# Optimization experiments

Measured on AMD Instinct MI355X. Metric: run time of the kernel, lower is better.

Reference implementation:

```python
import jax, jax.numpy as jnp
import numpy as np

B, DIM, H, W, HEAD = 8, 512, 32, 32, 8
DH = DIM // HEAD
N = H * W


def setup_inputs() -> dict:
    key = jax.random.key(0)
    ks = jax.random.split(key, 9)
    s = 0.05  # keep conv-weight scale modest so softmax logits are sane
    return {
        "x": jax.random.normal(ks[0], (B, DIM, H, W), jnp.float32),
        "wq_w": jax.random.normal(ks[1], (DIM, DIM), jnp.float32) * s,
        "wq_b": jax.random.normal(ks[2], (DIM,), jnp.float32) * s,
        "wk_w": jax.random.normal(ks[3], (DIM, DIM), jnp.float32) * s,
        "wk_b": jax.random.normal(ks[4], (DIM,), jnp.float32) * s,
        "wv_w": jax.random.normal(ks[5], (DIM, DIM), jnp.float32) * s,
        "wv_b": jax.random.normal(ks[6], (DIM,), jnp.float32) * s,
        "r_h": jax.random.normal(ks[7], (1, HEAD, DH, 1, H), jnp.float32),
        "r_w": jax.random.normal(ks[8], (1, HEAD, DH, W, 1), jnp.float32),
    }


def reference(x, wq_w, wq_b, wk_w, wk_b, wv_w, wv_b, r_h, r_w):
    b, dim, h, w = x.shape
    head = r_h.shape[1]
    dh = dim // head
    n = h * w

    def conv1x1(inp, wgt, bias):
        # 1x1 conv == channel-mixing matmul
        return jnp.einsum('bchw,oc->bohw', inp, wgt) + bias[None, :, None, None]

    q = conv1x1(x, wq_w, wq_b).reshape(b, head, dh, n).transpose(0, 1, 3, 2)  # [b,h,n,d]
    k = conv1x1(x, wk_w, wk_b).reshape(b, head, dh, n)                        # [b,h,d,n]
    v = conv1x1(x, wv_w, wv_b).reshape(b, head, dh, n)                        # [b,h,d,n]

    # relative position term: (1,head,dh,1,H)+(1,head,dh,W,1) -> (1,head,dh,W*H)
    r = (r_h + r_w).reshape(head, dh, n)

    content_position = jnp.einsum('bhnd,hdm->bhnm', q, r)
    content_content = jnp.einsum('bhnd,bhdm->bhnm', q, k)
    # faithful odd reduction: softmax over the whole flattened (head*n*n) per batch row
    energy = (content_content + content_position).reshape(b, -1)
    attention = jax.nn.softmax(energy, axis=-1).reshape(b, head, n, n)

    feature = jnp.einsum('bhdn,bhnm->bhdm', v, attention).reshape(b, dim, h, w)
    # AvgPool2d(kernel=2, stride=2)
    out = feature.reshape(b, dim, h // 2, 2, w // 2, 2).mean(axis=(3, 5))
    return out
```

## Files before the change

kernel.cpp:

```cpp
#include <hip/hip_runtime.h>
#include <hip/hip_bf16.h>
#include <math.h>

#define BB   8
#define DIMC 512
#define HEAD 8
#define DH   64
#define NN   1024
#define HW   32

typedef __attribute__((ext_vector_type(8))) __bf16 bf16x8;
typedef __attribute__((ext_vector_type(4))) float  f32x4;
typedef __attribute__((ext_vector_type(4))) short  short4v;

#define MFMA16(a, b, c) __builtin_amdgcn_mfma_f32_16x16x32_bf16((a), (b), (c), 0, 0, 0)

__device__ __forceinline__ f32x4 mfma_pv(short4v a, short4v b, f32x4 c) {
#if __has_builtin(__builtin_amdgcn_mfma_f32_16x16x16bf16_1k)
    return __builtin_amdgcn_mfma_f32_16x16x16bf16_1k(a, b, c, 0, 0, 0);
#else
    asm volatile("v_mfma_f32_16x16x16_bf16 %0, %1, %2, %0"
                 : "+v"(c) : "v"(a), "v"(b));
    return c;
#endif
}

__device__ __forceinline__ int SW(int row, int col) {
    return (row << 6) + (col ^ ((row & 7) << 3));
}

__device__ __forceinline__ unsigned short bfh(float v) {
    unsigned int u = __float_as_uint(v);
    return (unsigned short)((u + 0x7fffu + ((u >> 16) & 1u)) >> 16);
}
__device__ __forceinline__ float bf2f(unsigned short h) {
    return __uint_as_float(((unsigned int)h) << 16);
}

__global__ __launch_bounds__(256)
void prep_x(const float* __restrict__ x,
            unsigned short* __restrict__ XTh, unsigned short* __restrict__ XTl)
{
    const int tid = threadIdx.x;
    const int nt = blockIdx.x;
    const int ct = blockIdx.y;
    const int b  = blockIdx.z;
    const int c0 = ct << 6, n0 = nt << 6;

    __shared__ float XsT[64][68];

    #pragma unroll
    for (int p = 0; p < 4; ++p) {
        int idx = tid + (p << 8);
        int cr = idx >> 4;
        int nc4 = (idx & 15) << 2;
        float4 v = *(const float4*)&x[((size_t)b * DIMC + c0 + cr) * NN + n0 + nc4];
        XsT[nc4 + 0][cr] = v.x;
        XsT[nc4 + 1][cr] = v.y;
        XsT[nc4 + 2][cr] = v.z;
        XsT[nc4 + 3][cr] = v.w;
    }
    __syncthreads();
    #pragma unroll
    for (int p = 0; p < 4; ++p) {
        int idx = tid + (p << 8);
        int n = idx >> 4;
        int c4 = (idx & 15) << 2;
        float4 v = *(const float4*)&XsT[n][c4];
        float vv[4] = {v.x, v.y, v.z, v.w};
        union { unsigned short u[4]; uint2 w; } ph, pl;
        #pragma unroll
        for (int j = 0; j < 4; ++j) {
            unsigned short hh = bfh(vv[j]);
            ph.u[j] = hh;
            pl.u[j] = bfh(vv[j] - bf2f(hh));
        }
        size_t off = ((size_t)(b * NN + n0 + n)) * DIMC + c0 + c4;
        *(uint2*)&XTh[off] = ph.w;
        *(uint2*)&XTl[off] = pl.w;
    }
}

__global__ __launch_bounds__(256)
void prep_w(const float* __restrict__ wq, const float* __restrict__ wk,
            const float* __restrict__ wv,
            unsigned short* __restrict__ Wh, unsigned short* __restrict__ Wl)
{
    const int z = blockIdx.y;
    const float* src = (z == 0) ? wq : (z == 1) ? wk : wv;
    const size_t zb = (size_t)z * DIMC * DIMC;
    #pragma unroll
    for (int p = 0; p < 4; ++p) {
        size_t i = (size_t)blockIdx.x * 4096 + (p << 10) + (threadIdx.x << 2);
        float4 v = *(const float4*)&src[i];
        float vv[4] = {v.x, v.y, v.z, v.w};
        union { unsigned short u[4]; uint2 w; } ph, pl;
        #pragma unroll
        for (int j = 0; j < 4; ++j) {
            unsigned short hh = bfh(vv[j]);
            ph.u[j] = hh;
            pl.u[j] = bfh(vv[j] - bf2f(hh));
        }
        *(uint2*)&Wh[zb + i] = ph.w;
        *(uint2*)&Wl[zb + i] = pl.w;
    }
}

__global__ __launch_bounds__(256)
void qkv_gemm(const unsigned short* __restrict__ XTh, const unsigned short* __restrict__ XTl,
              const unsigned short* __restrict__ Wh, const unsigned short* __restrict__ Wl,
              const float* __restrict__ wq_b, const float* __restrict__ wk_b,
              const float* __restrict__ wv_b,
              const float* __restrict__ r_h, const float* __restrict__ r_w,
              unsigned short* __restrict__ Qh, unsigned short* __restrict__ Ql,
              unsigned short* __restrict__ Kh, unsigned short* __restrict__ Kl,
              unsigned short* __restrict__ Vh, unsigned short* __restrict__ Vl)
{
    const int tid = threadIdx.x;
    const int z = blockIdx.z, hd = blockIdx.y;
    const int gn = blockIdx.x << 7;
    const int b = gn >> 10, posb = gn & 1023;
    const int oB = hd << 6;
    const int lane = tid & 63, w = tid >> 6;

    __shared__ __align__(16) unsigned short sm[24576];
    unsigned short* Ah = sm;
    unsigned short* Al = sm + 4096;
    unsigned short* Bh = sm + 8192;
    unsigned short* Bl = sm + 16384;

    const float* bias = (z == 0) ? wq_b : (z == 1) ? wk_b : wv_b;
    const unsigned short* wsh = Wh + (size_t)z * DIMC * DIMC + (size_t)oB * DIMC;
    const unsigned short* wsl = Wl + (size_t)z * DIMC * DIMC + (size_t)oB * DIMC;
    const unsigned short* xth = XTh + ((size_t)(b * NN + posb)) * DIMC;
    const unsigned short* xtl = XTl + ((size_t)(b * NN + posb)) * DIMC;

    f32x4 acc[8];
    #pragma unroll
    for (int t = 0; t < 8; ++t) acc[t] = (f32x4){0.f, 0.f, 0.f, 0.f};

    for (int ks = 0; ks < 8; ++ks) {
        const int c0 = ks << 6;
        #pragma unroll
        for (int p = 0; p < 2; ++p) {
            int idx = (p << 8) + tid;
            int row = idx >> 3, col8 = (idx & 7) << 3;
            size_t g = (size_t)row * DIMC + c0 + col8;
            *(float4*)&Ah[SW(row, col8)] = *(const float4*)&wsh[g];
            *(float4*)&Al[SW(row, col8)] = *(const float4*)&wsl[g];
        }
        #pragma unroll
        for (int p = 0; p < 4; ++p) {
            int idx = (p << 8) + tid;
            int row = idx >> 3, col8 = (idx & 7) << 3;
            size_t g = (size_t)row * DIMC + c0 + col8;
            *(float4*)&Bh[SW(row, col8)] = *(const float4*)&xth[g];
            *(float4*)&Bl[SW(row, col8)] = *(const float4*)&xtl[g];
        }
        __syncthreads();

        const int ar = (w << 4) + (lane & 15);
        const int kc = (lane >> 4) << 3;
        bf16x8 ah[2], al[2];
        ah[0] = *(const bf16x8*)&Ah[SW(ar, kc)];
        ah[1] = *(const bf16x8*)&Ah[SW(ar, 32 + kc)];
        al[0] = *(const bf16x8*)&Al[SW(ar, kc)];
        al[1] = *(const bf16x8*)&Al[SW(ar, 32 + kc)];
        #pragma unroll
        for (int t = 0; t < 8; ++t) {
            int br = (t << 4) + (lane & 15);
            #pragma unroll
            for (int s = 0; s < 2; ++s) {
                bf16x8 xh = *(const bf16x8*)&Bh[SW(br, s * 32 + kc)];
                bf16x8 xl = *(const bf16x8*)&Bl[SW(br, s * 32 + kc)];
                acc[t] = MFMA16(ah[s], xh, acc[t]);
                acc[t] = MFMA16(ah[s], xl, acc[t]);
                acc[t] = MFMA16(al[s], xh, acc[t]);
            }
        }
        __syncthreads();
    }

    float* F = (float*)sm;
    #pragma unroll
    for (int t = 0; t < 8; ++t) {
        int n = (t << 4) + (lane & 15);
        #pragma unroll
        for (int r = 0; r < 4; ++r) {
            int o = (w << 4) + ((lane >> 4) << 2) + r;
            F[o * 132 + n] = acc[t][r];
        }
    }
    __syncthreads();

    const size_t bh = (size_t)(b * HEAD + hd);
    if (z != 2) {
        unsigned short* Dh = (z == 0) ? Qh : Kh;
        unsigned short* Dl = (z == 0) ? Ql : Kl;
        #pragma unroll
        for (int p = 0; p < 8; ++p) {
            int idx = (p << 8) + tid;
            int n = idx >> 4, d0 = (idx & 15) << 2;
            union { unsigned short u[4]; uint2 v; } ph, pl;
            #pragma unroll
            for (int i = 0; i < 4; ++i) {
                int d = d0 + i;
                float val = F[d * 132 + n] + bias[oB + d];
                if (z == 1) {
                    int m = posb + n;
                    val += r_h[(size_t)(oB + d) * HW + (m & 31)]
                         + r_w[(size_t)(oB + d) * HW + (m >> 5)];
                }
                unsigned short hh = bfh(val);
                ph.u[i] = hh;
                pl.u[i] = bfh(val - bf2f(hh));
            }
            size_t off = (((size_t)bh * NN + posb + n) << 6) + d0;
            *(uint2*)&Dh[off] = ph.v;
            *(uint2*)&Dl[off] = pl.v;
        }
    } else {
        #pragma unroll
        for (int p = 0; p < 8; ++p) {
            int idx = (p << 8) + tid;
            int d = idx >> 5, n0 = (idx & 31) << 2;
            float4 v = *(const float4*)&F[d * 132 + n0];
            float vv[4] = {v.x, v.y, v.z, v.w};
            float bia = bias[oB + d];
            union { unsigned short u[4]; uint2 w2; } ph, pl;
            #pragma unroll
            for (int j = 0; j < 4; ++j) {
                float val = vv[j] + bia;
                unsigned short hh = bfh(val);
                ph.u[j] = hh;
                pl.u[j] = bfh(val - bf2f(hh));
            }
            size_t off = (((size_t)bh << 6) + d) * NN + posb + n0;
            *(uint2*)&Vh[off] = ph.w2;
            *(uint2*)&Vl[off] = pl.w2;
        }
    }
}

__global__ __launch_bounds__(256, 4)
void stats_kernel(const unsigned short* __restrict__ Qh, const unsigned short* __restrict__ Ql,
                  const unsigned short* __restrict__ Kh, const unsigned short* __restrict__ Kl,
                  float* __restrict__ pstats)
{
    const int tid = threadIdx.x;
    const int mt = blockIdx.x, hd = blockIdx.y, b = blockIdx.z;
    const int bh = b * HEAD + hd;
    const int lane = tid & 63, w = tid >> 6;
    const int r0 = lane & 15, c0 = (lane >> 4) << 3;

    __shared__ float red[512];

    const unsigned short* kh = Kh + (((size_t)bh * NN + (mt << 6)) << 6);
    const unsigned short* kl = Kl + (((size_t)bh * NN + (mt << 6)) << 6);
    bf16x8 kfh[4][2], kfl[4][2];
    #pragma unroll
    for (int t = 0; t < 4; ++t)
        #pragma unroll
        for (int s = 0; s < 2; ++s) {
            int off = (((t << 4) + r0) << 6) + (s << 5) + c0;
            kfh[t][s] = *(const bf16x8*)&kh[off];
            kfl[t][s] = *(const bf16x8*)&kl[off];
        }

    const unsigned short* qh = Qh + (((size_t)bh * NN) << 6);
    const unsigned short* ql = Ql + (((size_t)bh * NN) << 6);

    float m_r = -1e30f, s_r = 0.f;

    for (int nt = 0; nt < 16; ++nt) {
        const int qrow = (nt << 6) + (w << 4) + r0;
        const size_t qb = ((size_t)qrow << 6) + c0;
        bf16x8 ah0 = *(const bf16x8*)&qh[qb];
        bf16x8 ah1 = *(const bf16x8*)&qh[qb + 32];
        bf16x8 al0 = *(const bf16x8*)&ql[qb];
        bf16x8 al1 = *(const bf16x8*)&ql[qb + 32];

        f32x4 sacc[4];
        #pragma unroll
        for (int t = 0; t < 4; ++t) sacc[t] = (f32x4){0.f, 0.f, 0.f, 0.f};
        #pragma unroll
        for (int t = 0; t < 4; ++t) {
            sacc[t] = MFMA16(ah0, kfh[t][0], sacc[t]);
            sacc[t] = MFMA16(ah0, kfl[t][0], sacc[t]);
            sacc[t] = MFMA16(al0, kfh[t][0], sacc[t]);
        }
        #pragma unroll
        for (int t = 0; t < 4; ++t) {
            sacc[t] = MFMA16(ah1, kfh[t][1], sacc[t]);
            sacc[t] = MFMA16(ah1, kfl[t][1], sacc[t]);
            sacc[t] = MFMA16(al1, kfh[t][1], sacc[t]);
        }

        float tmax = -1e30f;
        #pragma unroll
        for (int t = 0; t < 4; ++t)
            #pragma unroll
            for (int r = 0; r < 4; ++r) tmax = fmaxf(tmax, sacc[t][r]);
        float nm = fmaxf(m_r, tmax);
        s_r *= __expf(m_r - nm);
        float tt = 0.f;
        #pragma unroll
        for (int t = 0; t < 4; ++t)
            #pragma unroll
            for (int r = 0; r < 4; ++r) tt += __expf(sacc[t][r] - nm);
        s_r += tt;
        m_r = nm;
    }

    red[tid] = m_r;
    red[256 + tid] = s_r;
    __syncthreads();
    for (int off = 128; off > 0; off >>= 1) {
        if (tid < off) {
            float m2 = red[tid + off], s2 = red[256 + tid + off];
            float M = fmaxf(red[tid], m2);
            red[256 + tid] = red[256 + tid] * __expf(red[tid] - M) + s2 * __expf(m2 - M);
            red[tid] = M;
        }
        __syncthreads();
    }
    if (tid == 0) {
        pstats[((b << 7) + (hd << 4) + mt) * 2 + 0] = red[0];
        pstats[((b << 7) + (hd << 4) + mt) * 2 + 1] = red[256];
    }
}

__global__ __launch_bounds__(128)
void combine_kernel(const float* __restrict__ pstats, float* __restrict__ gstats)
{
    const int b = blockIdx.x, tid = threadIdx.x;
    __shared__ float rm[128], rs[128];
    rm[tid] = pstats[((b << 7) + tid) * 2 + 0];
    rs[tid] = pstats[((b << 7) + tid) * 2 + 1];
    __syncthreads();
    for (int off = 64; off > 0; off >>= 1) {
        if (tid < off) {
            float m2 = rm[tid + off], s2 = rs[tid + off];
            float M = fmaxf(rm[tid], m2);
            rs[tid] = rs[tid] * __expf(rm[tid] - M) + s2 * __expf(m2 - M);
            rm[tid] = M;
        }
        __syncthreads();
    }
    if (tid == 0) { gstats[b * 2] = rm[0]; gstats[b * 2 + 1] = rs[0]; }
}

__global__ __launch_bounds__(256, 2)
void pv_kernel(const unsigned short* __restrict__ Qh, const unsigned short* __restrict__ Ql,
               const unsigned short* __restrict__ Kh, const unsigned short* __restrict__ Kl,
               const unsigned short* __restrict__ Vh, const unsigned short* __restrict__ Vl,
               const float* __restrict__ gstats, float* __restrict__ out)
{
    const int tid = threadIdx.x;
    const int mt = blockIdx.x, hd = blockIdx.y, b = blockIdx.z;
    const int bh = b * HEAD + hd;
    const int lane = tid & 63, w = tid >> 6;
    const int r0 = lane & 15, c0 = (lane >> 4) << 3;

    __shared__ __align__(16) unsigned char smraw[2 * 64 * 65 * 4];
    unsigned short* Vsh = (unsigned short*)smraw;
    unsigned short* Vsl = Vsh + 4096;
    float* F0 = (float*)smraw;
    float* F1 = F0 + 64 * 65;

    const unsigned short* kh = Kh + (((size_t)bh * NN + (mt << 6)) << 6);
    const unsigned short* kl = Kl + (((size_t)bh * NN + (mt << 6)) << 6);
    bf16x8 kfh[4][2], kfl[4][2];
    #pragma unroll
    for (int t = 0; t < 4; ++t)
        #pragma unroll
        for (int s = 0; s < 2; ++s) {
            int off = (((t << 4) + r0) << 6) + (s << 5) + c0;
            kfh[t][s] = *(const bf16x8*)&kh[off];
            kfl[t][s] = *(const bf16x8*)&kl[off];
        }

    const unsigned short* qh = Qh + (((size_t)bh * NN) << 6);
    const unsigned short* ql = Ql + (((size_t)bh * NN) << 6);
    const unsigned short* vh = Vh + (((size_t)bh << 6) * NN);
    const unsigned short* vl = Vl + (((size_t)bh << 6) * NN);

    const float gmax = gstats[b * 2];
    const float ginv = 1.f / gstats[b * 2 + 1];

    f32x4 facc[4][4];
    #pragma unroll
    for (int u = 0; u < 4; ++u)
        #pragma unroll
        for (int t = 0; t < 4; ++t) facc[u][t] = (f32x4){0.f, 0.f, 0.f, 0.f};

    for (int nt = 0; nt < 16; ++nt) {
        const int nB = nt << 6;
        #pragma unroll
        for (int p = 0; p < 2; ++p) {
            int idx = (p << 8) + tid;
            int row = idx >> 3, c8 = (idx & 7) << 3;
            *(float4*)&Vsh[SW(row, c8)] = *(const float4*)&vh[(size_t)row * NN + nB + c8];
            *(float4*)&Vsl[SW(row, c8)] = *(const float4*)&vl[(size_t)row * NN + nB + c8];
        }
        const int qrow = nB + (w << 4) + r0;
        const size_t qb = ((size_t)qrow << 6) + c0;
        bf16x8 ah0 = *(const bf16x8*)&qh[qb];
        bf16x8 ah1 = *(const bf16x8*)&qh[qb + 32];
        bf16x8 al0 = *(const bf16x8*)&ql[qb];
        bf16x8 al1 = *(const bf16x8*)&ql[qb + 32];
        __syncthreads();

        f32x4 sacc[4];
        #pragma unroll
        for (int t = 0; t < 4; ++t) sacc[t] = (f32x4){0.f, 0.f, 0.f, 0.f};
        #pragma unroll
        for (int t = 0; t < 4; ++t) {
            sacc[t] = MFMA16(ah0, kfh[t][0], sacc[t]);
            sacc[t] = MFMA16(ah0, kfl[t][0], sacc[t]);
            sacc[t] = MFMA16(al0, kfh[t][0], sacc[t]);
        }
        #pragma unroll
        for (int t = 0; t < 4; ++t) {
            sacc[t] = MFMA16(ah1, kfh[t][1], sacc[t]);
            sacc[t] = MFMA16(ah1, kfl[t][1], sacc[t]);
            sacc[t] = MFMA16(al1, kfh[t][1], sacc[t]);
        }

        short4v pah[4], pal[4];
        #pragma unroll
        for (int t = 0; t < 4; ++t) {
            union { unsigned short u[4]; short4v v; } Ph, Pl;
            #pragma unroll
            for (int r = 0; r < 4; ++r) {
                float a = __expf(sacc[t][r] - gmax) * ginv;
                unsigned short hh = bfh(a);
                Ph.u[r] = hh;
                Pl.u[r] = bfh(a - bf2f(hh));
            }
            pah[t] = Ph.v;
            pal[t] = Pl.v;
        }

        const int vcol = (w << 4) + ((lane >> 4) << 2);
        #pragma unroll
        for (int u = 0; u < 4; ++u) {
            int vrow = (u << 4) + r0;
            short4v vah = *(const short4v*)&Vsh[SW(vrow, vcol)];
            short4v vbl = *(const short4v*)&Vsl[SW(vrow, vcol)];
            #pragma unroll
            for (int t = 0; t < 4; ++t) {
                facc[u][t] = mfma_pv(vah, pah[t], facc[u][t]);
                facc[u][t] = mfma_pv(vbl, pah[t], facc[u][t]);
                facc[u][t] = mfma_pv(vah, pal[t], facc[u][t]);
            }
        }
        __syncthreads();
    }

    const int fr = (lane >> 4) << 2;
    if (w < 2) {
        float* Fw = (w == 0) ? F0 : F1;
        #pragma unroll
        for (int u = 0; u < 4; ++u)
            #pragma unroll
            for (int t = 0; t < 4; ++t)
                #pragma unroll
                for (int r = 0; r < 4; ++r)
                    Fw[((u << 4) + fr + r) * 65 + (t << 4) + r0] = facc[u][t][r];
    }
    __syncthreads();
    if (w >= 2) {
        float* Fw = (w == 2) ? F0 : F1;
        #pragma unroll
        for (int u = 0; u < 4; ++u)
            #pragma unroll
            for (int t = 0; t < 4; ++t)
                #pragma unroll
                for (int r = 0; r < 4; ++r)
                    Fw[((u << 4) + fr + r) * 65 + (t << 4) + r0] += facc[u][t][r];
    }
    __syncthreads();
    #pragma unroll
    for (int q = 0; q < 4; ++q) {
        int idx = (tid << 2) + q;
        int d = idx >> 4, wo = idx & 15;
        int m0 = wo << 1;
        float v = 0.25f * ((F0[d * 65 + m0]      + F1[d * 65 + m0]) +
                           (F0[d * 65 + m0 + 1]  + F1[d * 65 + m0 + 1]) +
                           (F0[d * 65 + 32 + m0] + F1[d * 65 + 32 + m0]) +
                           (F0[d * 65 + 33 + m0] + F1[d * 65 + 33 + m0]));
        out[(((size_t)(b * DIMC + (hd << 6) + d) << 4) + mt) * 16 + wo] = v;
    }
}

extern "C" void kernel_launch(void* const* d_in, const int* in_sizes, int n_in,
                              void* d_out, int out_size, void* d_ws, size_t ws_size,
                              hipStream_t stream)
{
    const float* x    = (const float*)d_in[0];
    const float* wq_w = (const float*)d_in[1];
    const float* wq_b = (const float*)d_in[2];
    const float* wk_w = (const float*)d_in[3];
    const float* wk_b = (const float*)d_in[4];
    const float* wv_w = (const float*)d_in[5];
    const float* wv_b = (const float*)d_in[6];
    const float* r_h  = (const float*)d_in[7];
    const float* r_w  = (const float*)d_in[8];
    float* out = (float*)d_out;

    const size_t PRN = (size_t)BB * HEAD * NN * DH;
    const size_t WSZ = (size_t)3 * DIMC * DIMC;
    unsigned short* Qh  = (unsigned short*)d_ws;
    unsigned short* Ql  = Qh + PRN;
    unsigned short* Kh  = Ql + PRN;
    unsigned short* Kl  = Kh + PRN;
    unsigned short* Vh  = Kl + PRN;
    unsigned short* Vl  = Vh + PRN;
    unsigned short* XTh = Vl + PRN;
    unsigned short* XTl = XTh + PRN;
    unsigned short* Wh  = XTl + PRN;
    unsigned short* Wl  = Wh + WSZ;
    float* pstats = (float*)(Wl + WSZ);
    float* gstats = pstats + BB * 128 * 2;

    prep_x<<<dim3(16, 8, 8), 256, 0, stream>>>(x, XTh, XTl);
    prep_w<<<dim3(64, 3), 256, 0, stream>>>(wq_w, wk_w, wv_w, Wh, Wl);
    qkv_gemm<<<dim3(64, 8, 3), 256, 0, stream>>>(XTh, XTl, Wh, Wl,
                                                 wq_b, wk_b, wv_b, r_h, r_w,
                                                 Qh, Ql, Kh, Kl, Vh, Vl);
    stats_kernel<<<dim3(16, 8, 8), 256, 0, stream>>>(Qh, Ql, Kh, Kl, pstats);
    combine_kernel<<<dim3(8), 128, 0, stream>>>(pstats, gstats);
    pv_kernel<<<dim3(16, 8, 8), 256, 0, stream>>>(Qh, Ql, Kh, Kl, Vh, Vl, gstats, out);
}
```

Baseline: 256.9 us.

## Fuse softmax stats pass into PV pass with online rescaling and finalize

Replaces the separate stats pass and the PV pass, which both recomputed QK^T, with a single flash-style kernel. It keeps a per-wave running max, rescales the accumulators and writes an unnormalized pooled output plus per-block (max, sum). A small finalize kernel then applies the global softmax normalization per block. This removes one full QK^T recomputation and one read of Q/K, at the cost of extra rescale work, wave shuffles and an additional light kernel that writes pooled data into the reused XTh buffer.

```diff
diff --git a/kernel.cpp b/kernel.cpp
--- a/kernel.cpp
+++ b/kernel.cpp
@@ -242,10 +242,11 @@
     }
 }
 
-__global__ __launch_bounds__(256, 4)
-void stats_kernel(const unsigned short* __restrict__ Qh, const unsigned short* __restrict__ Ql,
-                  const unsigned short* __restrict__ Kh, const unsigned short* __restrict__ Kl,
-                  float* __restrict__ pstats)
+__global__ __launch_bounds__(256, 2)
+void flash_pv(const unsigned short* __restrict__ Qh, const unsigned short* __restrict__ Ql,
+              const unsigned short* __restrict__ Kh, const unsigned short* __restrict__ Kl,
+              const unsigned short* __restrict__ Vh, const unsigned short* __restrict__ Vl,
+              float* __restrict__ pooled, float* __restrict__ pstats)
 {
     const int tid = threadIdx.x;
     const int mt = blockIdx.x, hd = blockIdx.y, b = blockIdx.z;
@@ -253,7 +254,12 @@
     const int lane = tid & 63, w = tid >> 6;
     const int r0 = lane & 15, c0 = (lane >> 4) << 3;
 
-    __shared__ float red[512];
+    __shared__ __align__(16) unsigned char smraw[2 * 64 * 65 * 4];
+    unsigned short* Vsh = (unsigned short*)smraw;
+    unsigned short* Vsl = Vsh + 4096;
+    float* F0 = (float*)smraw;
+    float* F1 = F0 + 64 * 65;
+    __shared__ float bm[4], bs[4];
 
     const unsigned short* kh = Kh + (((size_t)bh * NN + (mt << 6)) << 6);
     const unsigned short* kl = Kl + (((size_t)bh * NN + (mt << 6)) << 6);
@@ -269,16 +275,34 @@
 
     const unsigned short* qh = Qh + (((size_t)bh * NN) << 6);
     const unsigned short* ql = Ql + (((size_t)bh * NN) << 6);
-
-    float m_r = -1e30f, s_r = 0.f;
+    const unsigned short* vh = Vh + (((size_t)bh << 6) * NN);
+    const unsigned short* vl = Vl + (((size_t)bh << 6) * NN);
+
+    float m_w = -1e30f;
+    float s_r = 0.f;
+
+    f32x4 facc[4][4];
+    #pragma unroll
+    for (int u = 0; u < 4; ++u)
+        #pragma unroll
+        for (int t = 0; t < 4; ++t) facc[u][t] = (f32x4){0.f, 0.f, 0.f, 0.f};
 
     for (int nt = 0; nt < 16; ++nt) {
-        const int qrow = (nt << 6) + (w << 4) + r0;
+        const int nB = nt << 6;
+        #pragma unroll
+        for (int p = 0; p < 2; ++p) {
+            int idx = (p << 8) + tid;
+            int row = idx >> 3, c8 = (idx & 7) << 3;
+            *(float4*)&Vsh[SW(row, c8)] = *(const float4*)&vh[(size_t)row * NN + nB + c8];
+            *(float4*)&Vsl[SW(row, c8)] = *(const float4*)&vl[(size_t)row * NN + nB + c8];
+        }
+        const int qrow = nB + (w << 4) + r0;
         const size_t qb = ((size_t)qrow << 6) + c0;
         bf16x8 ah0 = *(const bf16x8*)&qh[qb];
         bf16x8 ah1 = *(const bf16x8*)&qh[qb + 32];
         bf16x8 al0 = *(const bf16x8*)&ql[qb];
         bf16x8 al1 = *(const bf16x8*)&ql[qb + 32];
+        __syncthreads();
 
         f32x4 sacc[4];
         #pragma unroll
@@ -301,32 +325,101 @@
         for (int t = 0; t < 4; ++t)
             #pragma unroll
             for (int r = 0; r < 4; ++r) tmax = fmaxf(tmax, sacc[t][r]);
-        float nm = fmaxf(m_r, tmax);
-        s_r *= __expf(m_r - nm);
-        float tt = 0.f;
-        #pragma unroll
-        for (int t = 0; t < 4; ++t)
-            #pragma unroll
-            for (int r = 0; r < 4; ++r) tt += __expf(sacc[t][r] - nm);
-        s_r += tt;
-        m_r = nm;
-    }
-
-    red[tid] = m_r;
-    red[256 + tid] = s_r;
+        #pragma unroll
+        for (int off = 1; off < 64; off <<= 1)
+            tmax = fmaxf(tmax, __shfl_xor(tmax, off, 64));
+        if (tmax > m_w) {
+            float sc = __expf(m_w - tmax);
+            s_r *= sc;
+            #pragma unroll
+            for (int u = 0; u < 4; ++u)
+                #pragma unroll
+                for (int t = 0; t < 4; ++t) facc[u][t] *= sc;
+            m_w = tmax;
+        }
+
+        short4v pah[4], pal[4];
+        #pragma unroll
+        for (int t = 0; t < 4; ++t) {
+            union { unsigned short u[4]; short4v v; } Ph, Pl;
+            #pragma unroll
+            for (int r = 0; r < 4; ++r) {
+                float a = __expf(sacc[t][r] - m_w);
+                s_r += a;
+                unsigned short hh = bfh(a);
+                Ph.u[r] = hh;
+                Pl.u[r] = bfh(a - bf2f(hh));
+            }
+            pah[t] = Ph.v;
+            pal[t] = Pl.v;
+        }
+
+        const int vcol = (w << 4) + ((lane >> 4) << 2);
+        #pragma unroll
+        for (int u = 0; u < 4; ++u) {
+            int vrow = (u << 4) + r0;
+            short4v vah = *(const short4v*)&Vsh[SW(vrow, vcol)];
+            short4v vbl = *(const short4v*)&Vsl[SW(vrow, vcol)];
+            #pragma unroll
+            for (int t = 0; t < 4; ++t) {
+                facc[u][t] = mfma_pv(vah, pah[t], facc[u][t]);
+                facc[u][t] = mfma_pv(vbl, pah[t], facc[u][t]);
+                facc[u][t] = mfma_pv(vah, pal[t], facc[u][t]);
+            }
+        }
+        __syncthreads();
+    }
+
+    #pragma unroll
+    for (int off = 1; off < 64; off <<= 1) s_r += __shfl_xor(s_r, off, 64);
+    if (lane == 0) { bm[w] = m_w; bs[w] = s_r; }
     __syncthreads();
-    for (int off = 128; off > 0; off >>= 1) {
-        if (tid < off) {
-            float m2 = red[tid + off], s2 = red[256 + tid + off];
-            float M = fmaxf(red[tid], m2);
-            red[256 + tid] = red[256 + tid] * __expf(red[tid] - M) + s2 * __expf(m2 - M);
-            red[tid] = M;
-        }
-        __syncthreads();
-    }
+    const float m_B = fmaxf(fmaxf(bm[0], bm[1]), fmaxf(bm[2], bm[3]));
+    const float s_B = bs[0] * __expf(bm[0] - m_B) + bs[1] * __expf(bm[1] - m_B)
+                    + bs[2] * __expf(bm[2] - m_B) + bs[3] * __expf(bm[3] - m_B);
+    const float fsc = __expf(m_w - m_B);
+    #pragma unroll
+    for (int u = 0; u < 4; ++u)
+        #pragma unroll
+        for (int t = 0; t < 4; ++t) facc[u][t] *= fsc;
     if (tid == 0) {
-        pstats[((b << 7) + (hd << 4) + mt) * 2 + 0] = red[0];
-        pstats[((b << 7) + (hd << 4) + mt) * 2 + 1] = red[256];
+        pstats[((b << 7) + (hd << 4) + mt) * 2 + 0] = m_B;
+        pstats[((b << 7) + (hd << 4) + mt) * 2 + 1] = s_B;
+    }
+
+    const int fr = (lane >> 4) << 2;
+    if (w < 2) {
+        float* Fw = (w == 0) ? F0 : F1;
+        #pragma unroll
+        for (int u = 0; u < 4; ++u)
+            #pragma unroll
+            for (int t = 0; t < 4; ++t)
+                #pragma unroll
+                for (int r = 0; r < 4; ++r)
+                    Fw[((u << 4) + fr + r) * 65 + (t << 4) + r0] = facc[u][t][r];
+    }
+    __syncthreads();
+    if (w >= 2) {
+        float* Fw = (w == 2) ? F0 : F1;
+        #pragma unroll
+        for (int u = 0; u < 4; ++u)
+            #pragma unroll
+            for (int t = 0; t < 4; ++t)
+                #pragma unroll
+                for (int r = 0; r < 4; ++r)
+                    Fw[((u << 4) + fr + r) * 65 + (t << 4) + r0] += facc[u][t][r];
+    }
+    __syncthreads();
+    #pragma unroll
+    for (int q = 0; q < 4; ++q) {
+        int idx = (tid << 2) + q;
+        int d = idx >> 4, wo = idx & 15;
+        int m0 = wo << 1;
+        float v = 0.25f * ((F0[d * 65 + m0]      + F1[d * 65 + m0]) +
+                           (F0[d * 65 + m0 + 1]  + F1[d * 65 + m0 + 1]) +
+                           (F0[d * 65 + 32 + m0] + F1[d * 65 + 32 + m0]) +
+                           (F0[d * 65 + 33 + m0] + F1[d * 65 + 33 + m0]));
+        pooled[(((size_t)(b * DIMC + (hd << 6) + d) << 4) + mt) * 16 + wo] = v;
     }
 }
 
@@ -350,148 +443,21 @@
     if (tid == 0) { gstats[b * 2] = rm[0]; gstats[b * 2 + 1] = rs[0]; }
 }
 
-__global__ __launch_bounds__(256, 2)
-void pv_kernel(const unsigned short* __restrict__ Qh, const unsigned short* __restrict__ Ql,
-               const unsigned short* __restrict__ Kh, const unsigned short* __restrict__ Kl,
-               const unsigned short* __restrict__ Vh, const unsigned short* __restrict__ Vl,
-               const float* __restrict__ gstats, float* __restrict__ out)
-{
-    const int tid = threadIdx.x;
-    const int mt = blockIdx.x, hd = blockIdx.y, b = blockIdx.z;
-    const int bh = b * HEAD + hd;
-    const int lane = tid & 63, w = tid >> 6;
-    const int r0 = lane & 15, c0 = (lane >> 4) << 3;
-
-    __shared__ __align__(16) unsigned char smraw[2 * 64 * 65 * 4];
-    unsigned short* Vsh = (unsigned short*)smraw;
-    unsigned short* Vsl = Vsh + 4096;
-    float* F0 = (float*)smraw;
-    float* F1 = F0 + 64 * 65;
-
-    const unsigned short* kh = Kh + (((size_t)bh * NN + (mt << 6)) << 6);
-    const unsigned short* kl = Kl + (((size_t)bh * NN + (mt << 6)) << 6);
-    bf16x8 kfh[4][2], kfl[4][2];
-    #pragma unroll
-    for (int t = 0; t < 4; ++t)
-        #pragma unroll
-        for (int s = 0; s < 2; ++s) {
-            int off = (((t << 4) + r0) << 6) + (s << 5) + c0;
-            kfh[t][s] = *(const bf16x8*)&kh[off];
-            kfl[t][s] = *(const bf16x8*)&kl[off];
-        }
-
-    const unsigned short* qh = Qh + (((size_t)bh * NN) << 6);
-    const unsigned short* ql = Ql + (((size_t)bh * NN) << 6);
-    const unsigned short* vh = Vh + (((size_t)bh << 6) * NN);
-    const unsigned short* vl = Vl + (((size_t)bh << 6) * NN);
-
-    const float gmax = gstats[b * 2];
-    const float ginv = 1.f / gstats[b * 2 + 1];
-
-    f32x4 facc[4][4];
-    #pragma unroll
-    for (int u = 0; u < 4; ++u)
-        #pragma unroll
-        for (int t = 0; t < 4; ++t) facc[u][t] = (f32x4){0.f, 0.f, 0.f, 0.f};
-
-    for (int nt = 0; nt < 16; ++nt) {
-        const int nB = nt << 6;
-        #pragma unroll
-        for (int p = 0; p < 2; ++p) {
-            int idx = (p << 8) + tid;
-            int row = idx >> 3, c8 = (idx & 7) << 3;
-            *(float4*)&Vsh[SW(row, c8)] = *(const float4*)&vh[(size_t)row * NN + nB + c8];
-            *(float4*)&Vsl[SW(row, c8)] = *(const float4*)&vl[(size_t)row * NN + nB + c8];
-        }
-        const int qrow = nB + (w << 4) + r0;
-        const size_t qb = ((size_t)qrow << 6) + c0;
-        bf16x8 ah0 = *(const bf16x8*)&qh[qb];
-        bf16x8 ah1 = *(const bf16x8*)&qh[qb + 32];
-        bf16x8 al0 = *(const bf16x8*)&ql[qb];
-        bf16x8 al1 = *(const bf16x8*)&ql[qb + 32];
-        __syncthreads();
-
-        f32x4 sacc[4];
-        #pragma unroll
-        for (int t = 0; t < 4; ++t) sacc[t] = (f32x4){0.f, 0.f, 0.f, 0.f};
-        #pragma unroll
-        for (int t = 0; t < 4; ++t) {
-            sacc[t] = MFMA16(ah0, kfh[t][0], sacc[t]);
-            sacc[t] = MFMA16(ah0, kfl[t][0], sacc[t]);
-            sacc[t] = MFMA16(al0, kfh[t][0], sacc[t]);
-        }
-        #pragma unroll
-        for (int t = 0; t < 4; ++t) {
-            sacc[t] = MFMA16(ah1, kfh[t][1], sacc[t]);
-            sacc[t] = MFMA16(ah1, kfl[t][1], sacc[t]);
-            sacc[t] = MFMA16(al1, kfh[t][1], sacc[t]);
-        }
-
-        short4v pah[4], pal[4];
-        #pragma unroll
-        for (int t = 0; t < 4; ++t) {
-            union { unsigned short u[4]; short4v v; } Ph, Pl;
-            #pragma unroll
-            for (int r = 0; r < 4; ++r) {
-                float a = __expf(sacc[t][r] - gmax) * ginv;
-                unsigned short hh = bfh(a);
-                Ph.u[r] = hh;
-                Pl.u[r] = bfh(a - bf2f(hh));
-            }
-            pah[t] = Ph.v;
-            pal[t] = Pl.v;
-        }
-
-        const int vcol = (w << 4) + ((lane >> 4) << 2);
-        #pragma unroll
-        for (int u = 0; u < 4; ++u) {
-            int vrow = (u << 4) + r0;
-            short4v vah = *(const short4v*)&Vsh[SW(vrow, vcol)];
-            short4v vbl = *(const short4v*)&Vsl[SW(vrow, vcol)];
-            #pragma unroll
-            for (int t = 0; t < 4; ++t) {
-                facc[u][t] = mfma_pv(vah, pah[t], facc[u][t]);
-                facc[u][t] = mfma_pv(vbl, pah[t], facc[u][t]);
-                facc[u][t] = mfma_pv(vah, pal[t], facc[u][t]);
-            }
-        }
-        __syncthreads();
-    }
-
-    const int fr = (lane >> 4) << 2;
-    if (w < 2) {
-        float* Fw = (w == 0) ? F0 : F1;
-        #pragma unroll
-        for (int u = 0; u < 4; ++u)
-            #pragma unroll
-            for (int t = 0; t < 4; ++t)
-                #pragma unroll
-                for (int r = 0; r < 4; ++r)
-                    Fw[((u << 4) + fr + r) * 65 + (t << 4) + r0] = facc[u][t][r];
-    }
-    __syncthreads();
-    if (w >= 2) {
-        float* Fw = (w == 2) ? F0 : F1;
-        #pragma unroll
-        for (int u = 0; u < 4; ++u)
-            #pragma unroll
-            for (int t = 0; t < 4; ++t)
-                #pragma unroll
-                for (int r = 0; r < 4; ++r)
-                    Fw[((u << 4) + fr + r) * 65 + (t << 4) + r0] += facc[u][t][r];
-    }
-    __syncthreads();
-    #pragma unroll
-    for (int q = 0; q < 4; ++q) {
-        int idx = (tid << 2) + q;
-        int d = idx >> 4, wo = idx & 15;
-        int m0 = wo << 1;
-        float v = 0.25f * ((F0[d * 65 + m0]      + F1[d * 65 + m0]) +
-                           (F0[d * 65 + m0 + 1]  + F1[d * 65 + m0 + 1]) +
-                           (F0[d * 65 + 32 + m0] + F1[d * 65 + 32 + m0]) +
-                           (F0[d * 65 + 33 + m0] + F1[d * 65 + 33 + m0]));
-        out[(((size_t)(b * DIMC + (hd << 6) + d) << 4) + mt) * 16 + wo] = v;
-    }
+__global__ __launch_bounds__(256)
+void finalize(const float* __restrict__ pooled, const float* __restrict__ pstats,
+              const float* __restrict__ gstats, float* __restrict__ out)
+{
+    const int j = blockIdx.x * 256 + threadIdx.x;
+    const int e = j << 2;
+    const int mt = (e >> 4) & 15;
+    const int c  = e >> 8;
+    const int b  = c >> 9;
+    const int hd = (c >> 6) & 7;
+    const int sidx = (b << 7) + (hd << 4) + mt;
+    const float s = __expf(pstats[sidx * 2] - gstats[b * 2]) / gstats[b * 2 + 1];
+    float4 v = *(const float4*)&pooled[e];
+    v.x *= s; v.y *= s; v.z *= s; v.w *= s;
+    *(float4*)&out[e] = v;
 }
 
 extern "C" void kernel_launch(void* const* d_in, const int* in_sizes, int n_in,
@@ -523,13 +489,15 @@
     unsigned short* Wl  = Wh + WSZ;
     float* pstats = (float*)(Wl + WSZ);
     float* gstats = pstats + BB * 128 * 2;
+    float* pooled = (float*)XTh;
 
     prep_x<<<dim3(16, 8, 8), 256, 0, stream>>>(x, XTh, XTl);
     prep_w<<<dim3(64, 3), 256, 0, stream>>>(wq_w, wk_w, wv_w, Wh, Wl);
     qkv_gemm<<<dim3(64, 8, 3), 256, 0, stream>>>(XTh, XTl, Wh, Wl,
                                                  wq_b, wk_b, wv_b, r_h, r_w,
                                                  Qh, Ql, Kh, Kl, Vh, Vl);
-    stats_kernel<<<dim3(16, 8, 8), 256, 0, stream>>>(Qh, Ql, Kh, Kl, pstats);
+    flash_pv<<<dim3(16, 8, 8), 256, 0, stream>>>(Qh, Ql, Kh, Kl, Vh, Vl,
+                                                 pooled, pstats);
     combine_kernel<<<dim3(8), 128, 0, stream>>>(pstats, gstats);
-    pv_kernel<<<dim3(16, 8, 8), 256, 0, stream>>>(Qh, Ql, Kh, Kl, Vh, Vl, gstats, out);
-}
+    finalize<<<dim3(1024), 256, 0, stream>>>(pooled, pstats, gstats, out);
+}
```

Result: faster. 250.3 us (-2.6%).
